# Performance work log

Hardware: AMD Instinct MI355X
Metric: run time of the kernel (lower is better)

Reference implementation:

```python
import jax, jax.numpy as jnp
import numpy as np
from fractions import Fraction
from math import factorial, sqrt

MAX_SH = 2
BASE_L = [0, 1, 2]
MULT = 8
NUM_LAYERS = 2
N_NODES = 50000
N_EDGES = 1000000
FEAT_DIM = MULT * sum(2 * l + 1 for l in BASE_L)  # 72

# ---- exact SO(3) Clebsch-Gordan coefficients (e3nn convention, real SH basis) ----

def _su2_cg(j1, m1, j2, m2, j3, m3):
    if m3 != m1 + m2:
        return 0.0
    f = factorial
    vmin = max(-j1 + j2 + m3, -j1 + m1, 0)
    vmax = min(j2 + j3 + m1, j3 - j1 + j2, j3 + m3)
    C = (2 * j3 + 1) * Fraction(
        f(j3 + j1 - j2) * f(j3 - j1 + j2) * f(j1 + j2 - j3) * f(j3 + m3) * f(j3 - m3),
        f(j1 + j2 + j3 + 1) * f(j1 - m1) * f(j1 + m1) * f(j2 - m2) * f(j2 + m2))
    S = Fraction(0)
    for v in range(vmin, vmax + 1):
        S += (-1) ** (v + j2 + m2) * Fraction(
            f(j2 + j3 + m1 - v) * f(j1 - m1 + v),
            f(v) * f(j3 - j1 + j2 - v) * f(j3 + m3 - v) * f(v + j1 - j2 - m3))
    return sqrt(float(C)) * float(S)

def _su2_cg_table(j1, j2, j3):
    mat = np.zeros((2 * j1 + 1, 2 * j2 + 1, 2 * j3 + 1))
    if abs(j1 - j2) <= j3 <= j1 + j2:
        for m1 in range(-j1, j1 + 1):
            for m2 in range(-j2, j2 + 1):
                if abs(m1 + m2) <= j3:
                    mat[j1 + m1, j2 + m2, j3 + m1 + m2] = _su2_cg(j1, m1, j2, m2, j3, m1 + m2)
    return mat

def _real_to_complex(l):
    q = np.zeros((2 * l + 1, 2 * l + 1), dtype=np.complex128)
    for m in range(-l, 0):
        q[l + m, l + abs(m)] = 1 / sqrt(2)
        q[l + m, l - abs(m)] = -1j / sqrt(2)
    q[l, l] = 1.0
    for m in range(1, l + 1):
        q[l + m, l + abs(m)] = (-1) ** m / sqrt(2)
        q[l + m, l - abs(m)] = 1j * (-1) ** m / sqrt(2)
    return (-1j) ** l * q

def _so3_cg(l1, l2, l3):
    Q1, Q2, Q3 = _real_to_complex(l1), _real_to_complex(l2), _real_to_complex(l3)
    C = _su2_cg_table(l1, l2, l3).astype(np.complex128)
    C = np.einsum('ij,kl,mn,ikn->jlm', Q1, Q2, np.conj(Q3.T), C)
    assert np.abs(C.imag).max() < 1e-5
    return np.real(C)

def _build_tables():
    combos, cgs = [], []
    for deg in range(MAX_SH + 1):
        for ni, lni in enumerate(BASE_L):
            for no, lno in enumerate(BASE_L):
                if abs(deg - lni) <= lno <= deg + lni:
                    cg = _so3_cg(deg, lni, lno)
                    if np.abs(cg).sum() > 1e-10:
                        combos.append((deg, ni, no))
                        cgs.append(jnp.asarray(cg, dtype=jnp.float32))
    return combos, cgs

COMBOS, CGS = _build_tables()
NCOMB = len(COMBOS)  # 15 for max_sh=2, base_l=[0,1,2]


def setup_inputs() -> dict:
    key = jax.random.key(0)
    k = jax.random.split(key, 6)
    return {
        'node_irreps': jax.random.normal(k[0], (N_NODES, FEAT_DIM), jnp.float32),
        'edge_index': jax.random.randint(k[1], (2, N_EDGES), 0, N_NODES, jnp.int32),
        'sh0': jax.random.normal(k[2], (N_EDGES, 1), jnp.float32),
        'sh1': jax.random.normal(k[3], (N_EDGES, 3), jnp.float32),
        'sh2': jax.random.normal(k[4], (N_EDGES, 5), jnp.float32),
        'weights': jax.random.normal(k[5], (NUM_LAYERS, NCOMB, MULT, MULT), jnp.float32) * 0.1,
    }


def _apply_layer(node_feats, src, tgt, sh_list, w_layer):
    num_nodes = node_feats.shape[0]
    srcf = node_feats[src]  # [E, D] gather of source-node features
    # split into per-irrep blocks [E, mult, 2l+1] (channel-major layout, as in torch)
    blocks, o = [], 0
    for l in BASE_L:
        d = MULT * (2 * l + 1)
        blocks.append(srcf[:, o:o + d].reshape(-1, MULT, 2 * l + 1))
        o += d
    msgs = [jnp.zeros((src.shape[0], MULT, 2 * l + 1), node_feats.dtype) for l in BASE_L]
    for ci, (deg, ni, no) in enumerate(COMBOS):
        # per-edge CG tensor product: cg[i,j,k] * sh[e,i] * x[e,c,j] -> [e,c,k]
        base = jnp.einsum('ijk,ei,ecj->eck', CGS[ci], sh_list[deg], blocks[ni])
        # scalar weight per (in_channel c, out_channel o): W[ci] is [mult, mult]
        msgs[no] = msgs[no] + jnp.einsum('eck,co->eok', base, w_layer[ci])
    # scatter-add messages to target nodes, then concat irrep blocks
    aggs = [jax.ops.segment_sum(m.reshape(m.shape[0], -1), tgt, num_segments=num_nodes)
            for m in msgs]
    return jnp.concatenate(aggs, axis=1)


def reference(node_irreps, edge_index, sh0, sh1, sh2, weights):
    src, tgt = edge_index[0], edge_index[1]
    sh_list = (sh0, sh1, sh2)
    x = node_irreps
    for layer in range(NUM_LAYERS):
        x = _apply_layer(x, src, tgt, sh_list, weights[layer])
    return x
```

## Files before the change

### kernel.cpp

```cpp
#include <hip/hip_runtime.h>
#include <stdint.h>

#define DEVFN __device__ __forceinline__

namespace cgc {

constexpr double fact(int n){ double r = 1.0; for(int i = 2; i <= n; ++i) r *= (double)i; return r; }

constexpr double csqrt(double x){
  if(x <= 0.0) return 0.0;
  double g = x < 1.0 ? 1.0 : x;
  for(int i = 0; i < 64; ++i) g = 0.5*(g + x/g);
  return g;
}

constexpr double su2_cg(int j1,int m1,int j2,int m2,int j3,int m3){
  if(m1 + m2 != m3) return 0.0;
  int vmin = -j1 + j2 + m3;
  if(-j1 + m1 > vmin) vmin = -j1 + m1;
  if(0 > vmin) vmin = 0;
  int vmax = j2 + j3 + m1;
  if(j3 - j1 + j2 < vmax) vmax = j3 - j1 + j2;
  if(j3 + m3 < vmax) vmax = j3 + m3;
  double C = (double)(2*j3 + 1)
    * (fact(j3 + j1 - j2)*fact(j3 - j1 + j2)*fact(j1 + j2 - j3)*fact(j3 + m3)*fact(j3 - m3))
    / (fact(j1 + j2 + j3 + 1)*fact(j1 - m1)*fact(j1 + m1)*fact(j2 - m2)*fact(j2 + m2));
  double S = 0.0;
  for(int v = vmin; v <= vmax; ++v){
    double t = (fact(j2 + j3 + m1 - v)*fact(j1 - m1 + v))
      / (fact(v)*fact(j3 - j1 + j2 - v)*fact(j3 + m3 - v)*fact(v + j1 - j2 - m3));
    S += (((v + j2 + m2) & 1) ? -t : t);
  }
  return csqrt(C)*S;
}

struct C2 { double re; double im; };
constexpr C2 cmul(C2 a, C2 b){ return C2{a.re*b.re - a.im*b.im, a.re*b.im + a.im*b.re}; }

struct QM { C2 q[5][5]; };

constexpr QM rtc(int l){
  QM Q{};
  for(int a = 0; a < 5; ++a) for(int b = 0; b < 5; ++b) Q.q[a][b] = C2{0.0,0.0};
  const double inv = 1.0/csqrt(2.0);
  for(int m = -l; m < 0; ++m){
    Q.q[l+m][l-m] = C2{inv, 0.0};
    Q.q[l+m][l+m] = C2{0.0, -inv};
  }
  Q.q[l][l] = C2{1.0, 0.0};
  for(int m = 1; m <= l; ++m){
    const double sgn = (m & 1) ? -1.0 : 1.0;
    Q.q[l+m][l+m] = C2{sgn*inv, 0.0};
    Q.q[l+m][l-m] = C2{0.0, sgn*inv};
  }
  const C2 ph = (l == 0) ? C2{1.0,0.0} : (l == 1) ? C2{0.0,-1.0} : C2{-1.0,0.0};
  for(int a = 0; a < 2*l+1; ++a) for(int b = 0; b < 2*l+1; ++b) Q.q[a][b] = cmul(ph, Q.q[a][b]);
  return Q;
}

struct CG3 { double a[5][5][5]; };

constexpr CG3 so3(int l1,int l2,int l3){
  const QM Q1 = rtc(l1), Q2 = rtc(l2), Q3 = rtc(l3);
  const int d1 = 2*l1+1, d2 = 2*l2+1, d3 = 2*l3+1;
  CG3 R{};
  for(int a = 0; a < 5; ++a) for(int b = 0; b < 5; ++b) for(int c = 0; c < 5; ++c) R.a[a][b][c] = 0.0;
  for(int i = 0; i < d1; ++i) for(int k = 0; k < d2; ++k){
    const int m1 = i - l1, m2 = k - l2;
    if(m1 + m2 < -l3 || m1 + m2 > l3) continue;
    const int n = m1 + m2 + l3;
    const double c = su2_cg(l1, m1, l2, m2, l3, m1 + m2);
    if(c == 0.0) continue;
    for(int j = 0; j < d1; ++j){
      const C2 q1 = Q1.q[i][j]; if(q1.re == 0.0 && q1.im == 0.0) continue;
      for(int l = 0; l < d2; ++l){
        const C2 q2 = Q2.q[k][l]; if(q2.re == 0.0 && q2.im == 0.0) continue;
        const C2 q12 = cmul(q1, q2);
        for(int m = 0; m < d3; ++m){
          const C2 q3 = Q3.q[n][m]; if(q3.re == 0.0 && q3.im == 0.0) continue;
          const C2 p = cmul(q12, C2{q3.re, -q3.im});
          R.a[j][l][m] += c*p.re;
        }
      }
    }
  }
  return R;
}

constexpr int NCOMB = 15;
constexpr int CDEG[NCOMB] = {0,0,0, 1,1,1,1,1,1, 2,2,2,2,2,2};
constexpr int CNI [NCOMB] = {0,1,2, 0,1,1,1,2,2, 0,1,1,2,2,2};
constexpr int CNO [NCOMB] = {0,1,2, 1,0,1,2,1,2, 2,1,2,0,1,2};
constexpr int BOFF[NCOMB] = {0,1,4, 9,12,13,16,21,24, 29,34,37,42,43,46};
constexpr int BTOT = 51;

struct Tables { float cg[NCOMB][5][5][5]; };
constexpr Tables build(){
  Tables t{};
  for(int ci = 0; ci < NCOMB; ++ci){
    const CG3 r = so3(CDEG[ci], CNI[ci], CNO[ci]);
    for(int i = 0; i < 5; ++i) for(int j = 0; j < 5; ++j) for(int k = 0; k < 5; ++k)
      t.cg[ci][i][j][k] = (float)r.a[i][j][k];
  }
  return t;
}

}

__device__ constexpr cgc::Tables TAB = cgc::build();


template<int CI, int H>
DEVFN void contract_combo(const float (&M)[9][5], float (&bp)[cgc::BTOT]){
  constexpr int DEG = cgc::CDEG[CI];
  constexpr int NI  = cgc::CNI[CI];
  constexpr int NO  = cgc::CNO[CI];
  constexpr int DI = 2*DEG + 1, DJ = 2*NI + 1, DK = 2*NO + 1;
  constexpr int SHO = (DEG == 0) ? 0 : ((DEG == 1) ? 1 : 4);
  constexpr int XB  = (NI  == 0) ? 0 : ((NI  == 1) ? 1 : 4);
  constexpr int BO  = cgc::BOFF[CI];

#pragma unroll
  for(int k = 0; k < DK; ++k){
    float acc = 0.0f; bool any = false;
#pragma unroll
    for(int i = 0; i < DI; ++i){
#pragma unroll
      for(int j = 0; j < DJ; ++j){
        const int xj = XB + j;
        if(H == 0 && xj >= 4) continue;
        if(H == 1 && xj <  4) continue;
        const float cg = TAB.cg[CI][i][j][k];
        if(cg != 0.0f){ acc += cg * M[SHO + i][H ? (xj - 4) : xj]; any = true; }
      }
    }
    if(any) bp[BO + k] += acc;
  }
}

template<int H>
DEVFN void all_contract(const float (&M)[9][5], float (&bp)[cgc::BTOT]){
  contract_combo< 0,H>(M, bp);
  contract_combo< 1,H>(M, bp);
  contract_combo< 2,H>(M, bp);
  contract_combo< 3,H>(M, bp);
  contract_combo< 4,H>(M, bp);
  contract_combo< 5,H>(M, bp);
  contract_combo< 6,H>(M, bp);
  contract_combo< 7,H>(M, bp);
  contract_combo< 8,H>(M, bp);
  contract_combo< 9,H>(M, bp);
  contract_combo<10,H>(M, bp);
  contract_combo<11,H>(M, bp);
  contract_combo<12,H>(M, bp);
  contract_combo<13,H>(M, bp);
  contract_combo<14,H>(M, bp);
}

template<int CI>
DEVFN void combo_mix(const float (&B)[cgc::BTOT], float (&msg)[72],
                     const float* __restrict__ W, int c){
  constexpr int NO = cgc::CNO[CI];
  constexpr int DK = 2*NO + 1;
  constexpr int OO = (NO == 0) ? 0 : ((NO == 1) ? 8 : 32);
  constexpr int BO = cgc::BOFF[CI];
  const float* __restrict__ Wc = W + CI*64 + c*8;
#pragma unroll
  for(int o = 0; o < 8; ++o){
    const float w = Wc[o];
#pragma unroll
    for(int k = 0; k < DK; ++k) msg[OO + o*DK + k] += B[BO + k]*w;
  }
}

DEVFN void all_combo_mix(const float (&B)[cgc::BTOT], float (&msg)[72],
                         const float* __restrict__ W, int c){
  combo_mix< 0>(B, msg, W, c);
  combo_mix< 1>(B, msg, W, c);
  combo_mix< 2>(B, msg, W, c);
  combo_mix< 3>(B, msg, W, c);
  combo_mix< 4>(B, msg, W, c);
  combo_mix< 5>(B, msg, W, c);
  combo_mix< 6>(B, msg, W, c);
  combo_mix< 7>(B, msg, W, c);
  combo_mix< 8>(B, msg, W, c);
  combo_mix< 9>(B, msg, W, c);
  combo_mix<10>(B, msg, W, c);
  combo_mix<11>(B, msg, W, c);
  combo_mix<12>(B, msg, W, c);
  combo_mix<13>(B, msg, W, c);
  combo_mix<14>(B, msg, W, c);
}


__global__ __launch_bounds__(256)
void hist_kernel(const int* __restrict__ ei, int* __restrict__ cnt, int E){
  const int e = blockIdx.x*256 + threadIdx.x;
  if(e < E) atomicAdd(&cnt[ei[E + e]], 1);
}

__global__ __launch_bounds__(256)
void chunk_scan_kernel(const int* __restrict__ cnt, int* __restrict__ off,
                       int* __restrict__ chunkSum, int N){
  __shared__ int buf[1024];
  const int tid = threadIdx.x;
  const int base = blockIdx.x*1024;
  for(int j = tid; j < 1024; j += 256) buf[j] = (base + j < N) ? cnt[base + j] : 0;
  __syncthreads();
  if(tid == 0){
    int run = 0;
    for(int j = 0; j < 1024; ++j){ const int v = buf[j]; buf[j] = run; run += v; }
    chunkSum[blockIdx.x] = run;
  }
  __syncthreads();
  for(int j = tid; j < 1024; j += 256) if(base + j < N) off[base + j] = buf[j];
}

__global__ __launch_bounds__(64)
void chunk_offsets_kernel(int* __restrict__ chunkSum, int* __restrict__ offN, int C){
  if(threadIdx.x == 0 && blockIdx.x == 0){
    int run = 0;
    for(int c = 0; c < C; ++c){ const int v = chunkSum[c]; chunkSum[c] = run; run += v; }
    offN[0] = run;
  }
}

__global__ __launch_bounds__(256)
void apply_offsets_kernel(int* __restrict__ off, int* __restrict__ cursor,
                          const int* __restrict__ chunkSum, int N){
  const int i = blockIdx.x*256 + threadIdx.x;
  if(i < N){
    const int o = off[i] + chunkSum[i >> 10];
    off[i] = o;
    cursor[i] = o;
  }
}

template<bool B64>
__global__ __launch_bounds__(256)
void fill_kernel(const int* __restrict__ ei, int* __restrict__ cursor,
                 void* __restrict__ bucketv, int E){
  const int e = blockIdx.x*256 + threadIdx.x;
  if(e >= E) return;
  const int t = ei[E + e];
  const int p = atomicAdd(&cursor[t], 1);
  if constexpr(B64){
    ((uint2*)bucketv)[p] = make_uint2((uint32_t)e, (uint32_t)ei[e]);
  } else {
    ((int*)bucketv)[p] = e;
  }
}

__global__ __launch_bounds__(256)
void pack_x_v(const float* __restrict__ xin, float* __restrict__ xp, int N){
  const int idx = blockIdx.x*256 + threadIdx.x;
  if(idx >= N*8) return;
  const int n = idx >> 3, c = idx & 7;
  const float* row = xin + (size_t)n*72;
  const float4 a = make_float4(row[c],        row[8+3*c],  row[9+3*c],  row[10+3*c]);
  const float4 b = make_float4(row[32+5*c],   row[33+5*c], row[34+5*c], row[35+5*c]);
  const float4 d = make_float4(row[36+5*c],   0.f, 0.f, 0.f);
  float4* op = (float4*)(xp + (size_t)n*96 + c*12);
  op[0] = a; op[1] = b; op[2] = d;
}

__global__ __launch_bounds__(256)
void pack_all_v(const float* __restrict__ sh0, const float* __restrict__ sh1,
                const float* __restrict__ sh2, float* __restrict__ shp,
                const float* __restrict__ xin, float* __restrict__ xp,
                int E, int N){
  const int idx = blockIdx.x*256 + threadIdx.x;
  if(idx < E){
    const int e = idx;
    const float4 a = make_float4(sh0[e],      sh1[3*e],    sh1[3*e+1], sh1[3*e+2]);
    const float4 b = make_float4(sh2[5*e],    sh2[5*e+1],  sh2[5*e+2], sh2[5*e+3]);
    const float4 d = make_float4(sh2[5*e+4],  0.f, 0.f, 0.f);
    float4* op = (float4*)(shp + (size_t)e*12);
    op[0] = a; op[1] = b; op[2] = d;
    return;
  }
  const int r = idx - E;
  if(r >= N*8) return;
  const int n = r >> 3, c = r & 7;
  const float* row = xin + (size_t)n*72;
  const float4 a = make_float4(row[c],      row[8+3*c],  row[9+3*c],  row[10+3*c]);
  const float4 b = make_float4(row[32+5*c], row[33+5*c], row[34+5*c], row[35+5*c]);
  const float4 d = make_float4(row[36+5*c], 0.f, 0.f, 0.f);
  float4* op = (float4*)(xp + (size_t)n*96 + c*12);
  op[0] = a; op[1] = b; op[2] = d;
}


template<bool B64>
DEVFN void fetch_idx(const void* __restrict__ bktv, const int* __restrict__ ei,
                     int p, int& eid, int& src){
  if constexpr(B64){
    const uint2 b = ((const uint2*)bktv)[p];
    eid = (int)b.x; src = (int)b.y;
  } else {
    eid = ((const int*)bktv)[p];
    src = ei[eid];
  }
}

template<bool PX, bool PS>
DEVFN void load_edge_m(float (&sh)[9], float (&xs)[5],
                       int eid, int src, int c, int sub,
                       const float* __restrict__ x,  const float* __restrict__ xp,
                       const float* __restrict__ shp,
                       const float* __restrict__ sh0, const float* __restrict__ sh1,
                       const float* __restrict__ sh2){
  if constexpr(PS){
    const float4* sp = (const float4*)(shp + (size_t)eid*12);
    const float4 s0 = sp[0], s1 = sp[1];
    const float  s8 = shp[(size_t)eid*12 + 8];
    sh[0]=s0.x; sh[1]=s0.y; sh[2]=s0.z; sh[3]=s0.w;
    sh[4]=s1.x; sh[5]=s1.y; sh[6]=s1.z; sh[7]=s1.w;
    sh[8]=s8;
  } else {
    sh[0] = sh0[eid];
    sh[1] = sh1[3*eid+0]; sh[2] = sh1[3*eid+1]; sh[3] = sh1[3*eid+2];
    sh[4] = sh2[5*eid+0]; sh[5] = sh2[5*eid+1]; sh[6] = sh2[5*eid+2];
    sh[7] = sh2[5*eid+3]; sh[8] = sh2[5*eid+4];
  }
  if constexpr(PX){
    const float* base = xp + (size_t)src*96 + c*12;
    const float4 a = *(const float4*)(base + sub*4);
    const float  t8 = base[8];
    xs[0]=a.x; xs[1]=a.y; xs[2]=a.z; xs[3]=a.w;
    xs[4] = sub ? t8 : 0.0f;
  } else {
    const float* xrow = x + (size_t)src*72;
    if(sub == 0){
      xs[0] = xrow[c];
      xs[1] = xrow[8+3*c]; xs[2] = xrow[9+3*c]; xs[3] = xrow[10+3*c];
      xs[4] = 0.0f;
    } else {
#pragma unroll
      for(int k = 0; k < 5; ++k) xs[k] = xrow[32 + 5*c + k];
    }
  }
}

DEVFN void outer_acc(const float (&sh)[9], const float (&xs)[5], float (&M)[9][5]){
#pragma unroll
  for(int i = 0; i < 9; ++i)
#pragma unroll
    for(int j = 0; j < 5; ++j)
      M[i][j] += sh[i]*xs[j];
}

template<bool B64, bool PX, bool PS, bool PO>
__global__ __launch_bounds__(256)
void gather_m16(const float* __restrict__ x,
                const float* __restrict__ xp,
                const float* __restrict__ shp,
                const int*   __restrict__ ei,
                const float* __restrict__ sh0,
                const float* __restrict__ sh1,
                const float* __restrict__ sh2,
                const int*   __restrict__ off,
                const void*  __restrict__ bktv,
                const float* __restrict__ W,
                float* __restrict__ out,
                int N){
  const int t   = blockIdx.x*256 + threadIdx.x;
  const int g   = t >> 4;
  const int c   = t & 7;
  const int sub = (t >> 3) & 1;
  if(g >= N) return;

  const int pStart = off[g];
  const int pEnd   = off[g + 1];

  float M[9][5];
#pragma unroll
  for(int a = 0; a < 9; ++a)
#pragma unroll
    for(int b = 0; b < 5; ++b) M[a][b] = 0.0f;

  if(pStart < pEnd){
    float shA[9], xsA[5], shB[9], xsB[5], shC[9], xsC[5];
    int p = pStart;
    { int eid, src; fetch_idx<B64>(bktv, ei, p, eid, src);
      load_edge_m<PX,PS>(shA, xsA, eid, src, c, sub, x, xp, shp, sh0, sh1, sh2); }
    { const int pn = (p + 1 < pEnd) ? p + 1 : p;
      int eid, src; fetch_idx<B64>(bktv, ei, pn, eid, src);
      load_edge_m<PX,PS>(shB, xsB, eid, src, c, sub, x, xp, shp, sh0, sh1, sh2); }
    while(true){
      { const int pn = (p + 2 < pEnd) ? p + 2 : p;
        int eid, src; fetch_idx<B64>(bktv, ei, pn, eid, src);
        load_edge_m<PX,PS>(shC, xsC, eid, src, c, sub, x, xp, shp, sh0, sh1, sh2); }
      outer_acc(shA, xsA, M);
      ++p; if(p >= pEnd) break;
      { const int pn = (p + 2 < pEnd) ? p + 2 : p;
        int eid, src; fetch_idx<B64>(bktv, ei, pn, eid, src);
        load_edge_m<PX,PS>(shA, xsA, eid, src, c, sub, x, xp, shp, sh0, sh1, sh2); }
      outer_acc(shB, xsB, M);
      ++p; if(p >= pEnd) break;
      { const int pn = (p + 2 < pEnd) ? p + 2 : p;
        int eid, src; fetch_idx<B64>(bktv, ei, pn, eid, src);
        load_edge_m<PX,PS>(shB, xsB, eid, src, c, sub, x, xp, shp, sh0, sh1, sh2); }
      outer_acc(shC, xsC, M);
      ++p; if(p >= pEnd) break;
    }
  }

  float bp[cgc::BTOT];
#pragma unroll
  for(int i = 0; i < cgc::BTOT; ++i) bp[i] = 0.0f;
  if(sub == 0) all_contract<0>(M, bp);
  else         all_contract<1>(M, bp);

#pragma unroll
  for(int i = 0; i < cgc::BTOT; ++i) bp[i] += __shfl_xor(bp[i], 8);

  float msg[72];
#pragma unroll
  for(int d = 0; d < 72; ++d) msg[d] = 0.0f;
  all_combo_mix(bp, msg, W, c);

#pragma unroll
  for(int d = 0; d < 72; ++d){
    msg[d] += __shfl_xor(msg[d], 1);
    msg[d] += __shfl_xor(msg[d], 2);
    msg[d] += __shfl_xor(msg[d], 4);
  }

  if constexpr(PO){
    if(sub == 0){
      float4 w0, w1, w2;
      switch(c){
        case 0: w0 = make_float4(msg[0],msg[ 8],msg[ 9],msg[10]);
                w1 = make_float4(msg[32],msg[33],msg[34],msg[35]);
                w2 = make_float4(msg[36],0.f,0.f,0.f); break;
        case 1: w0 = make_float4(msg[1],msg[11],msg[12],msg[13]);
                w1 = make_float4(msg[37],msg[38],msg[39],msg[40]);
                w2 = make_float4(msg[41],0.f,0.f,0.f); break;
        case 2: w0 = make_float4(msg[2],msg[14],msg[15],msg[16]);
                w1 = make_float4(msg[42],msg[43],msg[44],msg[45]);
                w2 = make_float4(msg[46],0.f,0.f,0.f); break;
        case 3: w0 = make_float4(msg[3],msg[17],msg[18],msg[19]);
                w1 = make_float4(msg[47],msg[48],msg[49],msg[50]);
                w2 = make_float4(msg[51],0.f,0.f,0.f); break;
        case 4: w0 = make_float4(msg[4],msg[20],msg[21],msg[22]);
                w1 = make_float4(msg[52],msg[53],msg[54],msg[55]);
                w2 = make_float4(msg[56],0.f,0.f,0.f); break;
        case 5: w0 = make_float4(msg[5],msg[23],msg[24],msg[25]);
                w1 = make_float4(msg[57],msg[58],msg[59],msg[60]);
                w2 = make_float4(msg[61],0.f,0.f,0.f); break;
        case 6: w0 = make_float4(msg[6],msg[26],msg[27],msg[28]);
                w1 = make_float4(msg[62],msg[63],msg[64],msg[65]);
                w2 = make_float4(msg[66],0.f,0.f,0.f); break;
        default:w0 = make_float4(msg[7],msg[29],msg[30],msg[31]);
                w1 = make_float4(msg[67],msg[68],msg[69],msg[70]);
                w2 = make_float4(msg[71],0.f,0.f,0.f); break;
      }
      float4* op = (float4*)(out + (size_t)g*96 + c*12);
      op[0] = w0; op[1] = w1; op[2] = w2;
    }
  } else {
    if(sub == 0 && c == 0){
      float4* op = (float4*)(out + (size_t)g*72);
#pragma unroll
      for(int u = 0; u < 18; ++u){
        float4 v;
        v.x = msg[4*u + 0]; v.y = msg[4*u + 1];
        v.z = msg[4*u + 2]; v.w = msg[4*u + 3];
        op[u] = v;
      }
    }
  }
}


extern "C" void kernel_launch(void* const* d_in, const int* in_sizes, int n_in,
                              void* d_out, int out_size, void* d_ws, size_t ws_size,
                              hipStream_t stream){
  const float* node = (const float*)d_in[0];
  const int*   ei   = (const int*)  d_in[1];
  const float* sh0  = (const float*)d_in[2];
  const float* sh1  = (const float*)d_in[3];
  const float* sh2  = (const float*)d_in[4];
  const float* wts  = (const float*)d_in[5];
  float* out = (float*)d_out;

  const int E = in_sizes[1]/2;
  const int N = in_sizes[0]/72;
  const int C = (N + 1023)/1024;

  size_t baseI = (size_t)3*N + 65;
  baseI = (baseI + 3) & ~(size_t)3;
  const size_t availI = ws_size/4;
  const size_t t0Need = baseI + (size_t)2*E + (size_t)12*E + (size_t)96*N + (size_t)96*N;
  const size_t t1Need = baseI + (size_t)2*E + (size_t)96*N + (size_t)96*N;
  const int tier = (availI >= t0Need) ? 0 : (availI >= t1Need) ? 1 : 2;

  int* ws_i = (int*)d_ws;
  int* cnt      = ws_i;
  int* off      = ws_i + N;
  int* cursor   = ws_i + 2*N + 1;
  int* chunkSum = ws_i + 3*N + 1;
  size_t cur = baseI;
  void* bucket = (void*)(ws_i + cur); cur += (tier <= 1) ? (size_t)2*E : (size_t)E;
  float* shp = nullptr;
  float* xp1 = nullptr;
  float* xp2 = nullptr;
  float* inter = nullptr;
  if(tier == 0){ shp = (float*)(ws_i + cur); cur += (size_t)12*E; }
  if(tier <= 1){
    xp1 = (float*)(ws_i + cur); cur += (size_t)96*N;
    xp2 = (float*)(ws_i + cur); cur += (size_t)96*N;
  } else {
    inter = (float*)(ws_i + cur); cur += (size_t)72*N;
  }

  const int eBlocks = (E + 255)/256;
  const int nBlocks = (N + 255)/256;
  const int gBlocks = ((size_t)16*N + 255)/256;

  hipMemsetAsync(cnt, 0, (size_t)N*sizeof(int), stream);
  hist_kernel<<<eBlocks, 256, 0, stream>>>(ei, cnt, E);
  chunk_scan_kernel<<<C, 256, 0, stream>>>(cnt, off, chunkSum, N);
  chunk_offsets_kernel<<<1, 64, 0, stream>>>(chunkSum, off + N, C);
  apply_offsets_kernel<<<nBlocks, 256, 0, stream>>>(off, cursor, chunkSum, N);
  if(tier <= 1) fill_kernel<true ><<<eBlocks, 256, 0, stream>>>(ei, cursor, bucket, E);
  else          fill_kernel<false><<<eBlocks, 256, 0, stream>>>(ei, cursor, bucket, E);

  const float* w2 = wts + cgc::NCOMB*64;

  if(tier == 0){
    pack_all_v<<<((size_t)E + (size_t)8*N + 255)/256, 256, 0, stream>>>(
        sh0, sh1, sh2, shp, node, xp1, E, N);
    gather_m16<true,true,true,true ><<<gBlocks, 256, 0, stream>>>(
        nullptr, xp1, shp, ei, sh0, sh1, sh2, off, bucket, wts, xp2, N);
    gather_m16<true,true,true,false><<<gBlocks, 256, 0, stream>>>(
        nullptr, xp2, shp, ei, sh0, sh1, sh2, off, bucket, w2, out, N);
  } else if(tier == 1){
    pack_x_v<<<((size_t)8*N + 255)/256, 256, 0, stream>>>(node, xp1, N);
    gather_m16<true,true,false,true ><<<gBlocks, 256, 0, stream>>>(
        nullptr, xp1, nullptr, ei, sh0, sh1, sh2, off, bucket, wts, xp2, N);
    gather_m16<true,true,false,false><<<gBlocks, 256, 0, stream>>>(
        nullptr, xp2, nullptr, ei, sh0, sh1, sh2, off, bucket, w2, out, N);
  } else {
    gather_m16<false,false,false,false><<<gBlocks, 256, 0, stream>>>(
        node, nullptr, nullptr, ei, sh0, sh1, sh2, off, bucket, wts, inter, N);
    gather_m16<false,false,false,false><<<gBlocks, 256, 0, stream>>>(
        inter, nullptr, nullptr, ei, sh0, sh1, sh2, off, bucket, w2, out, N);
  }
}
```

Measured before the change: 386.8 us.

## Permute spherical harmonics into CSR order during bucket fill

The fill kernel now writes packed spherical harmonics and source indices directly at their sorted (by target) positions, so the gather kernels read per-edge data contiguously instead of through an edge-id indirection. This removes random sh reads in both layers and the separate bucket array, and shrinks per-edge index traffic to a single int. In exchange the fill step does scattered 48-byte writes, and the workspace layout for tier 0 changes.

After: 326.2 us. 1.19x faster.

```diff
diff --git a/kernel.cpp b/kernel.cpp
--- a/kernel.cpp
+++ b/kernel.cpp
@@ -192,220 +192,9 @@
   combo_mix<14>(B, msg, W, c);
 }
 
-
-__global__ __launch_bounds__(256)
-void hist_kernel(const int* __restrict__ ei, int* __restrict__ cnt, int E){
-  const int e = blockIdx.x*256 + threadIdx.x;
-  if(e < E) atomicAdd(&cnt[ei[E + e]], 1);
-}
-
-__global__ __launch_bounds__(256)
-void chunk_scan_kernel(const int* __restrict__ cnt, int* __restrict__ off,
-                       int* __restrict__ chunkSum, int N){
-  __shared__ int buf[1024];
-  const int tid = threadIdx.x;
-  const int base = blockIdx.x*1024;
-  for(int j = tid; j < 1024; j += 256) buf[j] = (base + j < N) ? cnt[base + j] : 0;
-  __syncthreads();
-  if(tid == 0){
-    int run = 0;
-    for(int j = 0; j < 1024; ++j){ const int v = buf[j]; buf[j] = run; run += v; }
-    chunkSum[blockIdx.x] = run;
-  }
-  __syncthreads();
-  for(int j = tid; j < 1024; j += 256) if(base + j < N) off[base + j] = buf[j];
-}
-
-__global__ __launch_bounds__(64)
-void chunk_offsets_kernel(int* __restrict__ chunkSum, int* __restrict__ offN, int C){
-  if(threadIdx.x == 0 && blockIdx.x == 0){
-    int run = 0;
-    for(int c = 0; c < C; ++c){ const int v = chunkSum[c]; chunkSum[c] = run; run += v; }
-    offN[0] = run;
-  }
-}
-
-__global__ __launch_bounds__(256)
-void apply_offsets_kernel(int* __restrict__ off, int* __restrict__ cursor,
-                          const int* __restrict__ chunkSum, int N){
-  const int i = blockIdx.x*256 + threadIdx.x;
-  if(i < N){
-    const int o = off[i] + chunkSum[i >> 10];
-    off[i] = o;
-    cursor[i] = o;
-  }
-}
-
-template<bool B64>
-__global__ __launch_bounds__(256)
-void fill_kernel(const int* __restrict__ ei, int* __restrict__ cursor,
-                 void* __restrict__ bucketv, int E){
-  const int e = blockIdx.x*256 + threadIdx.x;
-  if(e >= E) return;
-  const int t = ei[E + e];
-  const int p = atomicAdd(&cursor[t], 1);
-  if constexpr(B64){
-    ((uint2*)bucketv)[p] = make_uint2((uint32_t)e, (uint32_t)ei[e]);
-  } else {
-    ((int*)bucketv)[p] = e;
-  }
-}
-
-__global__ __launch_bounds__(256)
-void pack_x_v(const float* __restrict__ xin, float* __restrict__ xp, int N){
-  const int idx = blockIdx.x*256 + threadIdx.x;
-  if(idx >= N*8) return;
-  const int n = idx >> 3, c = idx & 7;
-  const float* row = xin + (size_t)n*72;
-  const float4 a = make_float4(row[c],        row[8+3*c],  row[9+3*c],  row[10+3*c]);
-  const float4 b = make_float4(row[32+5*c],   row[33+5*c], row[34+5*c], row[35+5*c]);
-  const float4 d = make_float4(row[36+5*c],   0.f, 0.f, 0.f);
-  float4* op = (float4*)(xp + (size_t)n*96 + c*12);
-  op[0] = a; op[1] = b; op[2] = d;
-}
-
-__global__ __launch_bounds__(256)
-void pack_all_v(const float* __restrict__ sh0, const float* __restrict__ sh1,
-                const float* __restrict__ sh2, float* __restrict__ shp,
-                const float* __restrict__ xin, float* __restrict__ xp,
-                int E, int N){
-  const int idx = blockIdx.x*256 + threadIdx.x;
-  if(idx < E){
-    const int e = idx;
-    const float4 a = make_float4(sh0[e],      sh1[3*e],    sh1[3*e+1], sh1[3*e+2]);
-    const float4 b = make_float4(sh2[5*e],    sh2[5*e+1],  sh2[5*e+2], sh2[5*e+3]);
-    const float4 d = make_float4(sh2[5*e+4],  0.f, 0.f, 0.f);
-    float4* op = (float4*)(shp + (size_t)e*12);
-    op[0] = a; op[1] = b; op[2] = d;
-    return;
-  }
-  const int r = idx - E;
-  if(r >= N*8) return;
-  const int n = r >> 3, c = r & 7;
-  const float* row = xin + (size_t)n*72;
-  const float4 a = make_float4(row[c],      row[8+3*c],  row[9+3*c],  row[10+3*c]);
-  const float4 b = make_float4(row[32+5*c], row[33+5*c], row[34+5*c], row[35+5*c]);
-  const float4 d = make_float4(row[36+5*c], 0.f, 0.f, 0.f);
-  float4* op = (float4*)(xp + (size_t)n*96 + c*12);
-  op[0] = a; op[1] = b; op[2] = d;
-}
-
-
-template<bool B64>
-DEVFN void fetch_idx(const void* __restrict__ bktv, const int* __restrict__ ei,
-                     int p, int& eid, int& src){
-  if constexpr(B64){
-    const uint2 b = ((const uint2*)bktv)[p];
-    eid = (int)b.x; src = (int)b.y;
-  } else {
-    eid = ((const int*)bktv)[p];
-    src = ei[eid];
-  }
-}
-
-template<bool PX, bool PS>
-DEVFN void load_edge_m(float (&sh)[9], float (&xs)[5],
-                       int eid, int src, int c, int sub,
-                       const float* __restrict__ x,  const float* __restrict__ xp,
-                       const float* __restrict__ shp,
-                       const float* __restrict__ sh0, const float* __restrict__ sh1,
-                       const float* __restrict__ sh2){
-  if constexpr(PS){
-    const float4* sp = (const float4*)(shp + (size_t)eid*12);
-    const float4 s0 = sp[0], s1 = sp[1];
-    const float  s8 = shp[(size_t)eid*12 + 8];
-    sh[0]=s0.x; sh[1]=s0.y; sh[2]=s0.z; sh[3]=s0.w;
-    sh[4]=s1.x; sh[5]=s1.y; sh[6]=s1.z; sh[7]=s1.w;
-    sh[8]=s8;
-  } else {
-    sh[0] = sh0[eid];
-    sh[1] = sh1[3*eid+0]; sh[2] = sh1[3*eid+1]; sh[3] = sh1[3*eid+2];
-    sh[4] = sh2[5*eid+0]; sh[5] = sh2[5*eid+1]; sh[6] = sh2[5*eid+2];
-    sh[7] = sh2[5*eid+3]; sh[8] = sh2[5*eid+4];
-  }
-  if constexpr(PX){
-    const float* base = xp + (size_t)src*96 + c*12;
-    const float4 a = *(const float4*)(base + sub*4);
-    const float  t8 = base[8];
-    xs[0]=a.x; xs[1]=a.y; xs[2]=a.z; xs[3]=a.w;
-    xs[4] = sub ? t8 : 0.0f;
-  } else {
-    const float* xrow = x + (size_t)src*72;
-    if(sub == 0){
-      xs[0] = xrow[c];
-      xs[1] = xrow[8+3*c]; xs[2] = xrow[9+3*c]; xs[3] = xrow[10+3*c];
-      xs[4] = 0.0f;
-    } else {
-#pragma unroll
-      for(int k = 0; k < 5; ++k) xs[k] = xrow[32 + 5*c + k];
-    }
-  }
-}
-
-DEVFN void outer_acc(const float (&sh)[9], const float (&xs)[5], float (&M)[9][5]){
-#pragma unroll
-  for(int i = 0; i < 9; ++i)
-#pragma unroll
-    for(int j = 0; j < 5; ++j)
-      M[i][j] += sh[i]*xs[j];
-}
-
-template<bool B64, bool PX, bool PS, bool PO>
-__global__ __launch_bounds__(256)
-void gather_m16(const float* __restrict__ x,
-                const float* __restrict__ xp,
-                const float* __restrict__ shp,
-                const int*   __restrict__ ei,
-                const float* __restrict__ sh0,
-                const float* __restrict__ sh1,
-                const float* __restrict__ sh2,
-                const int*   __restrict__ off,
-                const void*  __restrict__ bktv,
-                const float* __restrict__ W,
-                float* __restrict__ out,
-                int N){
-  const int t   = blockIdx.x*256 + threadIdx.x;
-  const int g   = t >> 4;
-  const int c   = t & 7;
-  const int sub = (t >> 3) & 1;
-  if(g >= N) return;
-
-  const int pStart = off[g];
-  const int pEnd   = off[g + 1];
-
-  float M[9][5];
-#pragma unroll
-  for(int a = 0; a < 9; ++a)
-#pragma unroll
-    for(int b = 0; b < 5; ++b) M[a][b] = 0.0f;
-
-  if(pStart < pEnd){
-    float shA[9], xsA[5], shB[9], xsB[5], shC[9], xsC[5];
-    int p = pStart;
-    { int eid, src; fetch_idx<B64>(bktv, ei, p, eid, src);
-      load_edge_m<PX,PS>(shA, xsA, eid, src, c, sub, x, xp, shp, sh0, sh1, sh2); }
-    { const int pn = (p + 1 < pEnd) ? p + 1 : p;
-      int eid, src; fetch_idx<B64>(bktv, ei, pn, eid, src);
-      load_edge_m<PX,PS>(shB, xsB, eid, src, c, sub, x, xp, shp, sh0, sh1, sh2); }
-    while(true){
-      { const int pn = (p + 2 < pEnd) ? p + 2 : p;
-        int eid, src; fetch_idx<B64>(bktv, ei, pn, eid, src);
-        load_edge_m<PX,PS>(shC, xsC, eid, src, c, sub, x, xp, shp, sh0, sh1, sh2); }
-      outer_acc(shA, xsA, M);
-      ++p; if(p >= pEnd) break;
-      { const int pn = (p + 2 < pEnd) ? p + 2 : p;
-        int eid, src; fetch_idx<B64>(bktv, ei, pn, eid, src);
-        load_edge_m<PX,PS>(shA, xsA, eid, src, c, sub, x, xp, shp, sh0, sh1, sh2); }
-      outer_acc(shB, xsB, M);
-      ++p; if(p >= pEnd) break;
-      { const int pn = (p + 2 < pEnd) ? p + 2 : p;
-        int eid, src; fetch_idx<B64>(bktv, ei, pn, eid, src);
-        load_edge_m<PX,PS>(shB, xsB, eid, src, c, sub, x, xp, shp, sh0, sh1, sh2); }
-      outer_acc(shC, xsC, M);
-      ++p; if(p >= pEnd) break;
-    }
-  }
-
+template<bool PO>
+DEVFN void node_epilogue(const float (&M)[9][5], const float* __restrict__ W,
+                         int c, int sub, int g, float* __restrict__ out){
   float bp[cgc::BTOT];
 #pragma unroll
   for(int i = 0; i < cgc::BTOT; ++i) bp[i] = 0.0f;
@@ -474,6 +263,272 @@
 }
 
 
+__global__ __launch_bounds__(256)
+void hist_kernel(const int* __restrict__ ei, int* __restrict__ cnt, int E){
+  const int e = blockIdx.x*256 + threadIdx.x;
+  if(e < E) atomicAdd(&cnt[ei[E + e]], 1);
+}
+
+__global__ __launch_bounds__(256)
+void chunk_scan_kernel(const int* __restrict__ cnt, int* __restrict__ off,
+                       int* __restrict__ chunkSum, int N){
+  __shared__ int buf[1024];
+  const int tid = threadIdx.x;
+  const int base = blockIdx.x*1024;
+  for(int j = tid; j < 1024; j += 256) buf[j] = (base + j < N) ? cnt[base + j] : 0;
+  __syncthreads();
+  if(tid == 0){
+    int run = 0;
+    for(int j = 0; j < 1024; ++j){ const int v = buf[j]; buf[j] = run; run += v; }
+    chunkSum[blockIdx.x] = run;
+  }
+  __syncthreads();
+  for(int j = tid; j < 1024; j += 256) if(base + j < N) off[base + j] = buf[j];
+}
+
+__global__ __launch_bounds__(64)
+void chunk_offsets_kernel(int* __restrict__ chunkSum, int* __restrict__ offN, int C){
+  if(threadIdx.x == 0 && blockIdx.x == 0){
+    int run = 0;
+    for(int c = 0; c < C; ++c){ const int v = chunkSum[c]; chunkSum[c] = run; run += v; }
+    offN[0] = run;
+  }
+}
+
+__global__ __launch_bounds__(256)
+void apply_offsets_kernel(int* __restrict__ off, int* __restrict__ cursor,
+                          const int* __restrict__ chunkSum, int N){
+  const int i = blockIdx.x*256 + threadIdx.x;
+  if(i < N){
+    const int o = off[i] + chunkSum[i >> 10];
+    off[i] = o;
+    cursor[i] = o;
+  }
+}
+
+__global__ __launch_bounds__(256)
+void fill_permute_kernel(const int* __restrict__ ei, int* __restrict__ cursor,
+                         int* __restrict__ srcs, float* __restrict__ shpp,
+                         const float* __restrict__ sh0, const float* __restrict__ sh1,
+                         const float* __restrict__ sh2, int E){
+  const int e = blockIdx.x*256 + threadIdx.x;
+  if(e >= E) return;
+  const int t = ei[E + e];
+  const int p = atomicAdd(&cursor[t], 1);
+  srcs[p] = ei[e];
+  const float4 a = make_float4(sh0[e],     sh1[3*e],   sh1[3*e+1], sh1[3*e+2]);
+  const float4 b = make_float4(sh2[5*e],   sh2[5*e+1], sh2[5*e+2], sh2[5*e+3]);
+  const float4 d = make_float4(sh2[5*e+4], 0.f, 0.f, 0.f);
+  float4* op = (float4*)(shpp + (size_t)p*12);
+  op[0] = a; op[1] = b; op[2] = d;
+}
+
+template<bool B64>
+__global__ __launch_bounds__(256)
+void fill_kernel(const int* __restrict__ ei, int* __restrict__ cursor,
+                 void* __restrict__ bucketv, int E){
+  const int e = blockIdx.x*256 + threadIdx.x;
+  if(e >= E) return;
+  const int t = ei[E + e];
+  const int p = atomicAdd(&cursor[t], 1);
+  if constexpr(B64){
+    ((uint2*)bucketv)[p] = make_uint2((uint32_t)e, (uint32_t)ei[e]);
+  } else {
+    ((int*)bucketv)[p] = e;
+  }
+}
+
+__global__ __launch_bounds__(256)
+void pack_x_v(const float* __restrict__ xin, float* __restrict__ xp, int N){
+  const int idx = blockIdx.x*256 + threadIdx.x;
+  if(idx >= N*8) return;
+  const int n = idx >> 3, c = idx & 7;
+  const float* row = xin + (size_t)n*72;
+  const float4 a = make_float4(row[c],        row[8+3*c],  row[9+3*c],  row[10+3*c]);
+  const float4 b = make_float4(row[32+5*c],   row[33+5*c], row[34+5*c], row[35+5*c]);
+  const float4 d = make_float4(row[36+5*c],   0.f, 0.f, 0.f);
+  float4* op = (float4*)(xp + (size_t)n*96 + c*12);
+  op[0] = a; op[1] = b; op[2] = d;
+}
+
+
+DEVFN void load_edge_p(float (&sh)[9], float (&xs)[5],
+                       int p, int c, int sub,
+                       const int* __restrict__ srcs,
+                       const float* __restrict__ shpp,
+                       const float* __restrict__ xp){
+  const float4* sp = (const float4*)(shpp + (size_t)p*12);
+  const float4 s0 = sp[0], s1 = sp[1];
+  const float  s8 = shpp[(size_t)p*12 + 8];
+  sh[0]=s0.x; sh[1]=s0.y; sh[2]=s0.z; sh[3]=s0.w;
+  sh[4]=s1.x; sh[5]=s1.y; sh[6]=s1.z; sh[7]=s1.w;
+  sh[8]=s8;
+  const int src = srcs[p];
+  const float* base = xp + (size_t)src*96 + c*12;
+  const float4 a = *(const float4*)(base + sub*4);
+  const float  t8 = base[8];
+  xs[0]=a.x; xs[1]=a.y; xs[2]=a.z; xs[3]=a.w;
+  xs[4] = sub ? t8 : 0.0f;
+}
+
+DEVFN void outer_acc(const float (&sh)[9], const float (&xs)[5], float (&M)[9][5]){
+#pragma unroll
+  for(int i = 0; i < 9; ++i)
+#pragma unroll
+    for(int j = 0; j < 5; ++j)
+      M[i][j] += sh[i]*xs[j];
+}
+
+template<bool PO>
+__global__ __launch_bounds__(256)
+void gather_perm(const float* __restrict__ xp,
+                 const float* __restrict__ shpp,
+                 const int*   __restrict__ srcs,
+                 const int*   __restrict__ off,
+                 const float* __restrict__ W,
+                 float* __restrict__ out,
+                 int N){
+  const int t   = blockIdx.x*256 + threadIdx.x;
+  const int g   = t >> 4;
+  const int c   = t & 7;
+  const int sub = (t >> 3) & 1;
+  if(g >= N) return;
+
+  const int pStart = off[g];
+  const int pEnd   = off[g + 1];
+
+  float M[9][5];
+#pragma unroll
+  for(int a = 0; a < 9; ++a)
+#pragma unroll
+    for(int b = 0; b < 5; ++b) M[a][b] = 0.0f;
+
+  if(pStart < pEnd){
+    float shA[9], xsA[5], shB[9], xsB[5], shC[9], xsC[5];
+    int p = pStart;
+    load_edge_p(shA, xsA, p, c, sub, srcs, shpp, xp);
+    { const int pn = (p + 1 < pEnd) ? p + 1 : p;
+      load_edge_p(shB, xsB, pn, c, sub, srcs, shpp, xp); }
+    while(true){
+      { const int pn = (p + 2 < pEnd) ? p + 2 : p;
+        load_edge_p(shC, xsC, pn, c, sub, srcs, shpp, xp); }
+      outer_acc(shA, xsA, M);
+      ++p; if(p >= pEnd) break;
+      { const int pn = (p + 2 < pEnd) ? p + 2 : p;
+        load_edge_p(shA, xsA, pn, c, sub, srcs, shpp, xp); }
+      outer_acc(shB, xsB, M);
+      ++p; if(p >= pEnd) break;
+      { const int pn = (p + 2 < pEnd) ? p + 2 : p;
+        load_edge_p(shB, xsB, pn, c, sub, srcs, shpp, xp); }
+      outer_acc(shC, xsC, M);
+      ++p; if(p >= pEnd) break;
+    }
+  }
+
+  node_epilogue<PO>(M, W, c, sub, g, out);
+}
+
+
+template<bool B64>
+DEVFN void fetch_idx(const void* __restrict__ bktv, const int* __restrict__ ei,
+                     int p, int& eid, int& src){
+  if constexpr(B64){
+    const uint2 b = ((const uint2*)bktv)[p];
+    eid = (int)b.x; src = (int)b.y;
+  } else {
+    eid = ((const int*)bktv)[p];
+    src = ei[eid];
+  }
+}
+
+template<bool PX>
+DEVFN void load_edge_m(float (&sh)[9], float (&xs)[5],
+                       int eid, int src, int c, int sub,
+                       const float* __restrict__ x,  const float* __restrict__ xp,
+                       const float* __restrict__ sh0, const float* __restrict__ sh1,
+                       const float* __restrict__ sh2){
+  sh[0] = sh0[eid];
+  sh[1] = sh1[3*eid+0]; sh[2] = sh1[3*eid+1]; sh[3] = sh1[3*eid+2];
+  sh[4] = sh2[5*eid+0]; sh[5] = sh2[5*eid+1]; sh[6] = sh2[5*eid+2];
+  sh[7] = sh2[5*eid+3]; sh[8] = sh2[5*eid+4];
+  if constexpr(PX){
+    const float* base = xp + (size_t)src*96 + c*12;
+    const float4 a = *(const float4*)(base + sub*4);
+    const float  t8 = base[8];
+    xs[0]=a.x; xs[1]=a.y; xs[2]=a.z; xs[3]=a.w;
+    xs[4] = sub ? t8 : 0.0f;
+  } else {
+    const float* xrow = x + (size_t)src*72;
+    if(sub == 0){
+      xs[0] = xrow[c];
+      xs[1] = xrow[8+3*c]; xs[2] = xrow[9+3*c]; xs[3] = xrow[10+3*c];
+      xs[4] = 0.0f;
+    } else {
+#pragma unroll
+      for(int k = 0; k < 5; ++k) xs[k] = xrow[32 + 5*c + k];
+    }
+  }
+}
+
+template<bool B64, bool PX, bool PO>
+__global__ __launch_bounds__(256)
+void gather_m16(const float* __restrict__ x,
+                const float* __restrict__ xp,
+                const int*   __restrict__ ei,
+                const float* __restrict__ sh0,
+                const float* __restrict__ sh1,
+                const float* __restrict__ sh2,
+                const int*   __restrict__ off,
+                const void*  __restrict__ bktv,
+                const float* __restrict__ W,
+                float* __restrict__ out,
+                int N){
+  const int t   = blockIdx.x*256 + threadIdx.x;
+  const int g   = t >> 4;
+  const int c   = t & 7;
+  const int sub = (t >> 3) & 1;
+  if(g >= N) return;
+
+  const int pStart = off[g];
+  const int pEnd   = off[g + 1];
+
+  float M[9][5];
+#pragma unroll
+  for(int a = 0; a < 9; ++a)
+#pragma unroll
+    for(int b = 0; b < 5; ++b) M[a][b] = 0.0f;
+
+  if(pStart < pEnd){
+    float shA[9], xsA[5], shB[9], xsB[5], shC[9], xsC[5];
+    int p = pStart;
+    { int eid, src; fetch_idx<B64>(bktv, ei, p, eid, src);
+      load_edge_m<PX>(shA, xsA, eid, src, c, sub, x, xp, sh0, sh1, sh2); }
+    { const int pn = (p + 1 < pEnd) ? p + 1 : p;
+      int eid, src; fetch_idx<B64>(bktv, ei, pn, eid, src);
+      load_edge_m<PX>(shB, xsB, eid, src, c, sub, x, xp, sh0, sh1, sh2); }
+    while(true){
+      { const int pn = (p + 2 < pEnd) ? p + 2 : p;
+        int eid, src; fetch_idx<B64>(bktv, ei, pn, eid, src);
+        load_edge_m<PX>(shC, xsC, eid, src, c, sub, x, xp, sh0, sh1, sh2); }
+      outer_acc(shA, xsA, M);
+      ++p; if(p >= pEnd) break;
+      { const int pn = (p + 2 < pEnd) ? p + 2 : p;
+        int eid, src; fetch_idx<B64>(bktv, ei, pn, eid, src);
+        load_edge_m<PX>(shA, xsA, eid, src, c, sub, x, xp, sh0, sh1, sh2); }
+      outer_acc(shB, xsB, M);
+      ++p; if(p >= pEnd) break;
+      { const int pn = (p + 2 < pEnd) ? p + 2 : p;
+        int eid, src; fetch_idx<B64>(bktv, ei, pn, eid, src);
+        load_edge_m<PX>(shB, xsB, eid, src, c, sub, x, xp, sh0, sh1, sh2); }
+      outer_acc(shC, xsC, M);
+      ++p; if(p >= pEnd) break;
+    }
+  }
+
+  node_epilogue<PO>(M, W, c, sub, g, out);
+}
+
+
 extern "C" void kernel_launch(void* const* d_in, const int* in_sizes, int n_in,
                               void* d_out, int out_size, void* d_ws, size_t ws_size,
                               hipStream_t stream){
@@ -492,7 +547,7 @@
   size_t baseI = (size_t)3*N + 65;
   baseI = (baseI + 3) & ~(size_t)3;
   const size_t availI = ws_size/4;
-  const size_t t0Need = baseI + (size_t)2*E + (size_t)12*E + (size_t)96*N + (size_t)96*N;
+  const size_t t0Need = baseI + (size_t)E + (size_t)12*E + (size_t)96*N + (size_t)96*N;
   const size_t t1Need = baseI + (size_t)2*E + (size_t)96*N + (size_t)96*N;
   const int tier = (availI >= t0Need) ? 0 : (availI >= t1Need) ? 1 : 2;
 
@@ -502,17 +557,26 @@
   int* cursor   = ws_i + 2*N + 1;
   int* chunkSum = ws_i + 3*N + 1;
   size_t cur = baseI;
-  void* bucket = (void*)(ws_i + cur); cur += (tier <= 1) ? (size_t)2*E : (size_t)E;
-  float* shp = nullptr;
+
+  int*   srcs  = nullptr;
+  float* shpp  = nullptr;
+  void*  bucket = nullptr;
   float* xp1 = nullptr;
   float* xp2 = nullptr;
   float* inter = nullptr;
-  if(tier == 0){ shp = (float*)(ws_i + cur); cur += (size_t)12*E; }
-  if(tier <= 1){
-    xp1 = (float*)(ws_i + cur); cur += (size_t)96*N;
-    xp2 = (float*)(ws_i + cur); cur += (size_t)96*N;
+
+  if(tier == 0){
+    srcs = (int*)(ws_i + cur);   cur += (size_t)E;
+    shpp = (float*)(ws_i + cur); cur += (size_t)12*E;
+    xp1  = (float*)(ws_i + cur); cur += (size_t)96*N;
+    xp2  = (float*)(ws_i + cur); cur += (size_t)96*N;
+  } else if(tier == 1){
+    bucket = (void*)(ws_i + cur); cur += (size_t)2*E;
+    xp1  = (float*)(ws_i + cur); cur += (size_t)96*N;
+    xp2  = (float*)(ws_i + cur); cur += (size_t)96*N;
   } else {
-    inter = (float*)(ws_i + cur); cur += (size_t)72*N;
+    bucket = (void*)(ws_i + cur); cur += (size_t)E;
+    inter  = (float*)(ws_i + cur); cur += (size_t)72*N;
   }
 
   const int eBlocks = (E + 255)/256;
@@ -524,28 +588,27 @@
   chunk_scan_kernel<<<C, 256, 0, stream>>>(cnt, off, chunkSum, N);
   chunk_offsets_kernel<<<1, 64, 0, stream>>>(chunkSum, off + N, C);
   apply_offsets_kernel<<<nBlocks, 256, 0, stream>>>(off, cursor, chunkSum, N);
-  if(tier <= 1) fill_kernel<true ><<<eBlocks, 256, 0, stream>>>(ei, cursor, bucket, E);
-  else          fill_kernel<false><<<eBlocks, 256, 0, stream>>>(ei, cursor, bucket, E);
 
   const float* w2 = wts + cgc::NCOMB*64;
 
   if(tier == 0){
-    pack_all_v<<<((size_t)E + (size_t)8*N + 255)/256, 256, 0, stream>>>(
-        sh0, sh1, sh2, shp, node, xp1, E, N);
-    gather_m16<true,true,true,true ><<<gBlocks, 256, 0, stream>>>(
-        nullptr, xp1, shp, ei, sh0, sh1, sh2, off, bucket, wts, xp2, N);
-    gather_m16<true,true,true,false><<<gBlocks, 256, 0, stream>>>(
-        nullptr, xp2, shp, ei, sh0, sh1, sh2, off, bucket, w2, out, N);
+    fill_permute_kernel<<<eBlocks, 256, 0, stream>>>(ei, cursor, srcs, shpp,
+                                                     sh0, sh1, sh2, E);
+    pack_x_v<<<((size_t)8*N + 255)/256, 256, 0, stream>>>(node, xp1, N);
+    gather_perm<true ><<<gBlocks, 256, 0, stream>>>(xp1, shpp, srcs, off, wts, xp2, N);
+    gather_perm<false><<<gBlocks, 256, 0, stream>>>(xp2, shpp, srcs, off, w2, out, N);
   } else if(tier == 1){
+    fill_kernel<true><<<eBlocks, 256, 0, stream>>>(ei, cursor, bucket, E);
     pack_x_v<<<((size_t)8*N + 255)/256, 256, 0, stream>>>(node, xp1, N);
-    gather_m16<true,true,false,true ><<<gBlocks, 256, 0, stream>>>(
-        nullptr, xp1, nullptr, ei, sh0, sh1, sh2, off, bucket, wts, xp2, N);
-    gather_m16<true,true,false,false><<<gBlocks, 256, 0, stream>>>(
-        nullptr, xp2, nullptr, ei, sh0, sh1, sh2, off, bucket, w2, out, N);
+    gather_m16<true,true,true ><<<gBlocks, 256, 0, stream>>>(
+        nullptr, xp1, ei, sh0, sh1, sh2, off, bucket, wts, xp2, N);
+    gather_m16<true,true,false><<<gBlocks, 256, 0, stream>>>(
+        nullptr, xp2, ei, sh0, sh1, sh2, off, bucket, w2, out, N);
   } else {
-    gather_m16<false,false,false,false><<<gBlocks, 256, 0, stream>>>(
-        node, nullptr, nullptr, ei, sh0, sh1, sh2, off, bucket, wts, inter, N);
-    gather_m16<false,false,false,false><<<gBlocks, 256, 0, stream>>>(
-        inter, nullptr, nullptr, ei, sh0, sh1, sh2, off, bucket, w2, out, N);
-  }
-}
+    fill_kernel<false><<<eBlocks, 256, 0, stream>>>(ei, cursor, bucket, E);
+    gather_m16<false,false,false><<<gBlocks, 256, 0, stream>>>(
+        node, nullptr, ei, sh0, sh1, sh2, off, bucket, wts, inter, N);
+    gather_m16<false,false,false><<<gBlocks, 256, 0, stream>>>(
+        inter, nullptr, ei, sh0, sh1, sh2, off, bucket, w2, out, N);
+  }
+}
```
